# Performance work log

Measured on AMD Instinct MI355X. Metric: run time of the kernel, lower is better.

The kernel has to match this reference:

```python
import jax, jax.numpy as jnp
import numpy as np

N = 100000       # nodes
E = 3200000      # edges (avg degree 32)
IN_C = 64        # in_channels
OUT_C = 10       # out_channels
F = 32           # hidden width of every GCNConv
L = 31           # number of GCNConv layers


def setup_inputs() -> dict:
    key = jax.random.key(0)
    ks = jax.random.split(key, 6)
    x = jax.random.normal(ks[0], (N, IN_C), dtype=jnp.float32)
    edge_index = jax.random.randint(ks[1], (2, E), 0, N, dtype=jnp.int64)
    W1 = jax.random.normal(ks[2], (IN_C, F), dtype=jnp.float32) * 0.1
    b1 = jnp.zeros((F,), dtype=jnp.float32)
    Wc = jax.random.normal(ks[3], (L, F, F), dtype=jnp.float32) * 0.1
    bc = jnp.zeros((L, F), dtype=jnp.float32)
    W2 = jax.random.normal(ks[4], (32 * F, OUT_C), dtype=jnp.float32) * 0.05
    b2 = jnp.zeros((OUT_C,), dtype=jnp.float32)
    return {"x": x, "edge_index": edge_index, "W1": W1, "b1": b1,
            "Wc": Wc, "bc": bc, "W2": W2, "b2": b2}


def mynorm(t):
    mn = t.min(axis=1, keepdims=True)
    mx = t.max(axis=1, keepdims=True)
    return 2.0 * (t - mn) / (mx - mn + 1e-8) - 1.0


def reference(x, edge_index, W1, b1, Wc, bc, W2, b2):
    src, dst = edge_index[0], edge_index[1]
    # GCN symmetric normalization with self-loops: deg = in-degree + 1
    deg = jax.ops.segment_sum(jnp.ones((E,), jnp.float32), dst, num_segments=N) + 1.0
    dis = jax.lax.rsqrt(deg)                       # [N]
    enorm = (dis[src] * dis[dst])[:, None]         # per-edge norm
    snorm = (dis * dis)[:, None]                   # self-loop norm

    def gcn(h, W, b):
        h = h @ W                                  # [N,32]
        agg = jax.ops.segment_sum(h[src] * enorm, dst, num_segments=N)
        return agg + snorm * h + b

    x0 = mynorm(jax.nn.relu(x @ W1 + b1))
    xs = [x0]
    for i in range(L):
        xs.append(gcn(xs[-1], Wc[i], bc[i]))
    norms = [mynorm(t) for t in xs]
    parts = [x0, xs[1]]                            # x0 and xx1 = x1 (raw)
    for i in range(2, 32):
        # quirk in original: index 16 uses raw x16, not a norm difference
        parts.append(xs[16] if i == 16 else norms[i] - norms[i - 2])
    feats = jnp.concatenate(parts, axis=1)         # [N, 32*32]
    return feats @ W2 + b2
```

## Files before the change

### kernel.cpp

```cpp
#include <hip/hip_runtime.h>


#define NB 4
#define BSHIFT 15
#define CSH 9
#define GSLACK 6152

__device__ __forceinline__ float shflx(float v, int m) { return __shfl_xor(v, m, 64); }

__global__ __launch_bounds__(1024) void k_chist(const int* __restrict__ dst, int E,
                                                int* __restrict__ gcnt, int G1) {
    __shared__ int lh[256];
    if (threadIdx.x < 256) lh[threadIdx.x] = 0;
    __syncthreads();
    int chunk = (E + gridDim.x - 1) / gridDim.x;
    int s0 = blockIdx.x * chunk, s1 = min(E, s0 + chunk);
    for (int e = s0 + threadIdx.x; e < s1; e += 1024)
        atomicAdd(&lh[dst[e] >> CSH], 1);
    __syncthreads();
    if (threadIdx.x < G1 && lh[threadIdx.x])
        atomicAdd(&gcnt[threadIdx.x], lh[threadIdx.x]);
}

__global__ void k_cscan(const int* __restrict__ gcnt, int* __restrict__ gptr,
                        int* __restrict__ gcur, int G1, int E) {
    __shared__ int s[256];
    int t = threadIdx.x;
    int v = (t < G1) ? gcnt[t] : 0;
    s[t] = v;
    __syncthreads();
    for (int off = 1; off < 256; off <<= 1) {
        int tv = (t >= off) ? s[t - off] : 0;
        __syncthreads();
        s[t] += tv;
        __syncthreads();
    }
    if (t < G1) { int ex = s[t] - v; gptr[t] = ex; gcur[t] = ex; }
    if (t == 0) gptr[G1] = E;
}

__global__ __launch_bounds__(1024) void k_cscatter(const int* __restrict__ src,
                                                   const int* __restrict__ dst, int E,
                                                   int* __restrict__ gcur,
                                                   int* __restrict__ tmp, int G1) {
    __shared__ int lh[256], lc[256];
    if (threadIdx.x < 256) lh[threadIdx.x] = 0;
    __syncthreads();
    int chunk = (E + gridDim.x - 1) / gridDim.x;
    int s0 = blockIdx.x * chunk, s1 = min(E, s0 + chunk);
    for (int e = s0 + threadIdx.x; e < s1; e += 1024)
        atomicAdd(&lh[dst[e] >> CSH], 1);
    __syncthreads();
    if (threadIdx.x < G1) {
        int c = lh[threadIdx.x];
        lc[threadIdx.x] = c ? atomicAdd(&gcur[threadIdx.x], c) : 0;
    }
    __syncthreads();
    for (int e = s0 + threadIdx.x; e < s1; e += 1024) {
        int d = dst[e];
        int pos = atomicAdd(&lc[d >> CSH], 1);
        tmp[pos] = src[e] | ((d & ((1 << CSH) - 1)) << 17);
    }
}

__global__ __launch_bounds__(256) void k_build(const int* __restrict__ tmp,
                                               const int* __restrict__ gptr,
                                               int* __restrict__ rp4,
                                               int* __restrict__ csr,
                                               float* __restrict__ dis,
                                               int* __restrict__ gend,
                                               int N, int M) {
    __shared__ int h[2048];
    __shared__ int c[2048];
    __shared__ int s[256];
    int g = blockIdx.x;
    int gb = gptr[g], ge = gptr[g + 1];
    int gbP = ((gb + 3) & ~3) + g * GSLACK;
    int t = threadIdx.x;
#pragma unroll
    for (int k = 0; k < 8; ++k) h[t * 8 + k] = 0;
    __syncthreads();
    for (int e = gb + t; e < ge; e += 256) {
        int w = tmp[e];
        int srcv = w & 0x1FFFF, ldst = w >> 17;
        atomicAdd(&h[ldst * NB + (srcv >> BSHIFT)], 1);
    }
    __syncthreads();
    int base8 = t * 8;
    int loc[8], sumP = 0;
#pragma unroll
    for (int k = 0; k < 8; ++k) { loc[k] = h[base8 + k]; sumP += (loc[k] + 3) & ~3; }
    s[t] = sumP;
    __syncthreads();
    for (int off = 1; off < 256; off <<= 1) {
        int tv = (t >= off) ? s[t - off] : 0;
        __syncthreads();
        s[t] += tv;
        __syncthreads();
    }
    int runP = s[t] - sumP;
    int rowbase = g * 2048;
#pragma unroll
    for (int k = 0; k < 8; ++k) {
        int i = base8 + k;
        int abs0 = gbP + runP;
        c[i] = abs0;
        int ig = rowbase + i;
        if (ig <= M) rp4[ig] = abs0;
        int lp = (loc[k] + 3) & ~3;
        for (int j = loc[k]; j < lp; ++j) csr[abs0 + j] = N;
        runP += lp;
    }
    __syncthreads();
    for (int e = gb + t; e < ge; e += 256) {
        int w = tmp[e];
        int srcv = w & 0x1FFFF, ldst = w >> 17;
        int pos = atomicAdd(&c[ldst * NB + (srcv >> BSHIFT)], 1);
        csr[pos] = srcv;
    }
    int nodebase = g << CSH;
    for (int ln = t; ln < (1 << CSH); ln += 256) {
        int n = nodebase + ln;
        if (n < N) {
            int d = h[ln * NB] + h[ln * NB + 1] + h[ln * NB + 2] + h[ln * NB + 3];
            dis[n] = rsqrtf((float)d + 1.0f);
        }
    }
    if (t == 0) gend[g] = gbP + s[255];
    if (g == gridDim.x - 1 && t == 0) rp4[M] = gbP + s[255];
}

__global__ void k_mnorm(const float* __restrict__ W2, float* __restrict__ Mn,
                        float* __restrict__ Rw, float* __restrict__ C0) {
    int idx = blockIdx.x * blockDim.x + threadIdx.x;
    if (idx >= 32 * 32 * 10) return;
    int c = idx % 32, o = (idx / 32) % 10, j = idx / 320;
    float v = 0.f;
    if (j >= 2 && j != 16) v += W2[(32 * j + c) * 10 + o];
    if (j <= 29 && j != 14) v -= W2[(32 * (j + 2) + c) * 10 + o];
    Mn[idx] = v;
    float rw = (j == 0 || j == 1 || j == 16) ? W2[(32 * j + c) * 10 + o] : 0.f;
    Rw[idx] = rw;
    if (j == 0) C0[idx] = v + rw;
}

__global__ __launch_bounds__(256) void k_x0(
    const float* __restrict__ x, const float* __restrict__ W1, const float* __restrict__ b1,
    const float* __restrict__ b2, const float* __restrict__ C0,
    const float* __restrict__ dis, float* __restrict__ hs, float* __restrict__ out, int N)
{
    __shared__ float Wt[32 * 68];
    __shared__ float xs[8 * 64];
    __shared__ float bs[32];
    __shared__ float Cs[10 * 36];
    __shared__ float xmat[8 * 36];
    int t = threadIdx.x;
    for (int i = t; i < 2048; i += 256) {
        int k = i >> 5, cc = i & 31;
        Wt[cc * 68 + k] = W1[i];
    }
    for (int i = t; i < 320; i += 256) {
        int o = i >> 5, cc = i & 31;
        Cs[o * 36 + cc] = C0[i];
    }
    if (t < 32) bs[t] = b1[t];
    if (blockIdx.x == 0 && t < 32) hs[(size_t)N * 32 + t] = 0.f;
    int base = blockIdx.x * 8;
    {
        int nf2 = (min(N - base, 8)) * 32;
        const float2* x2 = (const float2*)(x + (size_t)base * 64);
        float2* xs2 = (float2*)xs;
        for (int i = t; i < nf2; i += 256) xs2[i] = x2[i];
    }
    __syncthreads();

    int node8 = t >> 5, c = t & 31;
    int n = base + node8;
    bool nvalid = (n < N);

    const float4* xs4 = (const float4*)(xs + node8 * 64);
    const float4* Wt4 = (const float4*)(Wt + c * 68);
    float acc = bs[c];
#pragma unroll
    for (int k4 = 0; k4 < 16; ++k4) {
        float4 xv = xs4[k4];
        float4 wv = Wt4[k4];
        acc += xv.x * wv.x + xv.y * wv.y + xv.z * wv.z + xv.w * wv.w;
    }
    acc = fmaxf(acc, 0.f);

    float mn = acc, mx = acc;
#pragma unroll
    for (int m = 1; m <= 16; m <<= 1) { mn = fminf(mn, shflx(mn, m)); mx = fmaxf(mx, shflx(mx, m)); }
    float x0 = 2.f * (acc - mn) / (mx - mn + 1e-8f) - 1.f;
    if (nvalid) {
        float dn = dis[n];
        hs[(size_t)n * 32 + c] = dn * x0;
        xmat[node8 * 36 + c] = x0;
    }
    __syncthreads();

    if (t < 80) {
        int n8 = t / 10, o = t - n8 * 10;
        int no = base + n8;
        if (no < N) {
            const float4* xr = (const float4*)(xmat + n8 * 36);
            const float4* cr = (const float4*)(Cs + o * 36);
            float a = 0.f;
#pragma unroll
            for (int k = 0; k < 8; ++k) {
                float4 xv = xr[k];
                float4 cv = cr[k];
                a += xv.x * cv.x + xv.y * cv.y + xv.z * cv.z + xv.w * cv.w;
            }
            out[(size_t)no * 10 + o] = b2[o] + a;
        }
    }
}

__global__ __launch_bounds__(256) void k_gcn(
    const float4* __restrict__ hs_in, float4* __restrict__ hs_out,
    const float* __restrict__ dis, const int* __restrict__ rp4,
    const int* __restrict__ csr, const int* __restrict__ gend,
    const float* __restrict__ W, const float* __restrict__ b,
    const float* __restrict__ Mn, const float* __restrict__ Rw,
    float* __restrict__ out, int N, int israw)
{
    __shared__ float Ws[1024];
    __shared__ float bs[32];
    __shared__ float Ms[320];
    __shared__ float Rs[320];
    for (int i = threadIdx.x; i < 1024; i += 256) Ws[i] = W[i];
    for (int i = threadIdx.x; i < 320; i += 256) { Ms[i] = Mn[i]; Rs[i] = Rw[i]; }
    if (threadIdx.x < 32) bs[threadIdx.x] = b[threadIdx.x];
    if (blockIdx.x == 0 && threadIdx.x < 8)
        hs_out[(size_t)N * 8 + threadIdx.x] = make_float4(0.f, 0.f, 0.f, 0.f);
    __syncthreads();

    int lane = threadIdx.x & 63;
    int q = lane & 7;
    int i8 = lane >> 3;
    int wave = threadIdx.x >> 6;
    int n = blockIdx.x * 32 + wave * 8 + i8;
    bool valid = (n < N);
    int nn = valid ? n : (N - 1);

    float4 acc = hs_in[(size_t)nn * 8 + q];

    int rbase = nn * NB;
    int rs = rp4[rbase];
    int e3 = ((nn & ((1 << CSH) - 1)) == ((1 << CSH) - 1)) ? gend[nn >> CSH]
                                                          : rp4[rbase + 4];
    const int4* csr4 = (const int4*)csr;
    int4 idx = csr4[rs >> 2];
    for (int p = 0; p < NB; ++p) {
        int re = (p == NB - 1) ? e3 : rp4[rbase + p + 1];
        for (int e = rs; e < re; e += 4) {
            int s0 = idx.x, s1 = idx.y, s2 = idx.z, s3 = idx.w;
            idx = csr4[(e + 4) >> 2];
            float4 v0 = hs_in[(size_t)(s0 * 8 + q)];
            float4 v1 = hs_in[(size_t)(s1 * 8 + q)];
            float4 v2 = hs_in[(size_t)(s2 * 8 + q)];
            float4 v3 = hs_in[(size_t)(s3 * 8 + q)];
            acc.x += v0.x; acc.y += v0.y; acc.z += v0.z; acc.w += v0.w;
            acc.x += v1.x; acc.y += v1.y; acc.z += v1.z; acc.w += v1.w;
            acc.x += v2.x; acc.y += v2.y; acc.z += v2.z; acc.w += v2.w;
            acc.x += v3.x; acc.y += v3.y; acc.z += v3.z; acc.w += v3.w;
        }
        rs = re;
        if (p < NB - 1) __syncthreads();
    }

    float dn = dis[nn];
    float4 g = make_float4(dn * acc.x, dn * acc.y, dn * acc.z, dn * acc.w);

    const float4* W4 = (const float4*)Ws;
    float4 bb = ((const float4*)bs)[q];
    float4 xn = bb;
    int ibase = lane & 0x38;
#pragma unroll
    for (int kp = 0; kp < 8; ++kp) {
        int sl = ibase | kp;
        float gx = __shfl(g.x, sl, 64);
        float gy = __shfl(g.y, sl, 64);
        float gz = __shfl(g.z, sl, 64);
        float gw = __shfl(g.w, sl, 64);
        float4 w0 = W4[(kp * 4 + 0) * 8 + q];
        float4 w1 = W4[(kp * 4 + 1) * 8 + q];
        float4 w2 = W4[(kp * 4 + 2) * 8 + q];
        float4 w3 = W4[(kp * 4 + 3) * 8 + q];
        xn.x += gx * w0.x + gy * w1.x + gz * w2.x + gw * w3.x;
        xn.y += gx * w0.y + gy * w1.y + gz * w2.y + gw * w3.y;
        xn.z += gx * w0.z + gy * w1.z + gz * w2.z + gw * w3.z;
        xn.w += gx * w0.w + gy * w1.w + gz * w2.w + gw * w3.w;
    }

    if (valid)
        hs_out[(size_t)n * 8 + q] = make_float4(dn * xn.x, dn * xn.y, dn * xn.z, dn * xn.w);

    float mn = fminf(fminf(xn.x, xn.y), fminf(xn.z, xn.w));
    float mx = fmaxf(fmaxf(xn.x, xn.y), fmaxf(xn.z, xn.w));
#pragma unroll
    for (int m = 1; m <= 4; m <<= 1) { mn = fminf(mn, shflx(mn, m)); mx = fmaxf(mx, shflx(mx, m)); }
    float sc = 2.f / (mx - mn + 1e-8f);
    float4 nr = make_float4((xn.x - mn) * sc - 1.f, (xn.y - mn) * sc - 1.f,
                            (xn.z - mn) * sc - 1.f, (xn.w - mn) * sc - 1.f);

    const float4* M4 = (const float4*)Ms;
    const float4* R4 = (const float4*)Rs;
    float outA = 0.f, outB = 0.f;
#pragma unroll
    for (int o = 0; o < 10; ++o) {
        float4 m4 = M4[o * 8 + q];
        float t = nr.x * m4.x + nr.y * m4.y + nr.z * m4.z + nr.w * m4.w;
        if (israw) {
            float4 r4 = R4[o * 8 + q];
            t += xn.x * r4.x + xn.y * r4.y + xn.z * r4.z + xn.w * r4.w;
        }
        t += shflx(t, 1); t += shflx(t, 2); t += shflx(t, 4);
        if (o == q) outA = t;
        if (o == 8 + q) outB = t;
    }
    if (valid) {
        out[n * 10 + q] += outA;
        if (q < 2) out[n * 10 + 8 + q] += outB;
    }
}

extern "C" void kernel_launch(void* const* d_in, const int* in_sizes, int n_in,
                              void* d_out, int out_size, void* d_ws, size_t ws_size,
                              hipStream_t stream)
{
    const float* x  = (const float*)d_in[0];
    const int*   ei = (const int*)d_in[1];
    const float* W1 = (const float*)d_in[2];
    const float* b1 = (const float*)d_in[3];
    const float* Wc = (const float*)d_in[4];
    const float* bc = (const float*)d_in[5];
    const float* W2 = (const float*)d_in[6];
    const float* b2 = (const float*)d_in[7];
    float* out = (float*)d_out;

    const int N = in_sizes[0] / 64;
    const int E = in_sizes[1] / 2;
    const int M = N * NB;
    const int G1 = (N + (1 << CSH) - 1) >> CSH;
    const int* src = ei;
    const int* dst = ei + E;

    char* ws = (char*)d_ws;
    size_t off = 0;
    auto alloc = [&](size_t bytes) -> void* {
        void* p = ws + off;
        off = (off + bytes + 255) & ~size_t(255);
        return p;
    };
    int*   gcnt    = (int*)alloc(256 * 4);
    int*   gptr    = (int*)alloc(257 * 4);
    int*   gcur    = (int*)alloc(256 * 4);
    int*   rp4     = (int*)alloc((size_t)(M + 1) * 4);
    float* dis     = (float*)alloc((size_t)N * 4);
    int*   gend    = (int*)alloc(256 * 4);
    int*   tmp     = (int*)alloc((size_t)E * 4);
    int*   csr     = (int*)alloc(((size_t)E + (size_t)G1 * GSLACK + 64) * 4);
    float* hs_a    = (float*)alloc((size_t)(N + 1) * 32 * 4);
    float* hs_b    = (float*)alloc((size_t)(N + 1) * 32 * 4);
    float* Mn      = (float*)alloc(32 * 32 * 10 * 4);
    float* Rw      = (float*)alloc(32 * 32 * 10 * 4);
    float* C0      = (float*)alloc(320 * 4);

    hipMemsetAsync(gcnt, 0, 256 * 4, stream);
    k_chist<<<256, 1024, 0, stream>>>(dst, E, gcnt, G1);
    k_cscan<<<1, 256, 0, stream>>>(gcnt, gptr, gcur, G1, E);
    k_cscatter<<<256, 1024, 0, stream>>>(src, dst, E, gcur, tmp, G1);
    k_build<<<G1, 256, 0, stream>>>(tmp, gptr, rp4, csr, dis, gend, N, M);
    k_mnorm<<<(32 * 32 * 10 + 255) / 256, 256, 0, stream>>>(W2, Mn, Rw, C0);

    const int gb0 = (N + 7) / 8;
    k_x0<<<gb0, 256, 0, stream>>>(x, W1, b1, b2, C0, dis, hs_a, out, N);

    const int gb = (N + 31) / 32;
    float* hin = hs_a; float* hout = hs_b;
    for (int j = 1; j <= 31; ++j) {
        int israw = (j == 1 || j == 16) ? 1 : 0;
        k_gcn<<<gb, 256, 0, stream>>>((const float4*)hin, (float4*)hout, dis, rp4,
                                      csr, gend,
                                      Wc + (size_t)(j - 1) * 1024,
                                      bc + (size_t)(j - 1) * 32,
                                      Mn + (size_t)j * 320,
                                      Rw + (size_t)j * 320,
                                      out, N, israw);
        float* t = hin; hin = hout; hout = t;
    }
}
```

Baseline: 1.879 ms.

## Reorder CSR by source bucket and balance edge gathers across lanes per wave

```diff
diff --git a/kernel.cpp b/kernel.cpp
--- a/kernel.cpp
+++ b/kernel.cpp
@@ -83,7 +83,7 @@
     for (int e = gb + t; e < ge; e += 256) {
         int w = tmp[e];
         int srcv = w & 0x1FFFF, ldst = w >> 17;
-        atomicAdd(&h[ldst * NB + (srcv >> BSHIFT)], 1);
+        atomicAdd(&h[(srcv >> BSHIFT) * (1 << CSH) + ldst], 1);
     }
     __syncthreads();
     int base8 = t * 8;
@@ -105,29 +105,29 @@
         int i = base8 + k;
         int abs0 = gbP + runP;
         c[i] = abs0;
-        int ig = rowbase + i;
-        if (ig <= M) rp4[ig] = abs0;
+        rp4[rowbase + i] = abs0;
         int lp = (loc[k] + 3) & ~3;
-        for (int j = loc[k]; j < lp; ++j) csr[abs0 + j] = N;
+        int lb = i & ((1 << CSH) - 1);
+        int padw = (lb << 17) | N;
+        for (int j = loc[k]; j < lp; ++j) csr[abs0 + j] = padw;
         runP += lp;
     }
     __syncthreads();
     for (int e = gb + t; e < ge; e += 256) {
         int w = tmp[e];
         int srcv = w & 0x1FFFF, ldst = w >> 17;
-        int pos = atomicAdd(&c[ldst * NB + (srcv >> BSHIFT)], 1);
-        csr[pos] = srcv;
+        int pos = atomicAdd(&c[(srcv >> BSHIFT) * (1 << CSH) + ldst], 1);
+        csr[pos] = w;
     }
     int nodebase = g << CSH;
     for (int ln = t; ln < (1 << CSH); ln += 256) {
         int n = nodebase + ln;
         if (n < N) {
-            int d = h[ln * NB] + h[ln * NB + 1] + h[ln * NB + 2] + h[ln * NB + 3];
+            int d = h[ln] + h[512 + ln] + h[1024 + ln] + h[1536 + ln];
             dis[n] = rsqrtf((float)d + 1.0f);
         }
     }
     if (t == 0) gend[g] = gbP + s[255];
-    if (g == gridDim.x - 1 && t == 0) rp4[M] = gbP + s[255];
 }
 
 __global__ void k_mnorm(const float* __restrict__ W2, float* __restrict__ Mn,
@@ -218,6 +218,16 @@
     }
 }
 
+#define FLUSHP() do { if (cur >= 0) { \
+    atomicAdd(&wsc[wave][cur][(q << 2)    ], part.x); \
+    atomicAdd(&wsc[wave][cur][(q << 2) + 1], part.y); \
+    atomicAdd(&wsc[wave][cur][(q << 2) + 2], part.z); \
+    atomicAdd(&wsc[wave][cur][(q << 2) + 3], part.w); } } while (0)
+#define EDGE(wrd) do { int slot = ((wrd) >> 17) - l0; \
+    if (slot != cur) { FLUSHP(); cur = slot; part = make_float4(0.f, 0.f, 0.f, 0.f); } \
+    float4 v = hs_in[(size_t)((((wrd) & 0x1FFFF)) * 8 + q)]; \
+    part.x += v.x; part.y += v.y; part.z += v.z; part.w += v.w; } while (0)
+
 __global__ __launch_bounds__(256) void k_gcn(
     const float4* __restrict__ hs_in, float4* __restrict__ hs_out,
     const float* __restrict__ dis, const int* __restrict__ rp4,
@@ -230,9 +240,11 @@
     __shared__ float bs[32];
     __shared__ float Ms[320];
     __shared__ float Rs[320];
+    __shared__ float wsc[4][8][32];
     for (int i = threadIdx.x; i < 1024; i += 256) Ws[i] = W[i];
     for (int i = threadIdx.x; i < 320; i += 256) { Ms[i] = Mn[i]; Rs[i] = Rw[i]; }
     if (threadIdx.x < 32) bs[threadIdx.x] = b[threadIdx.x];
+    ((float4*)wsc)[threadIdx.x] = make_float4(0.f, 0.f, 0.f, 0.f);
     if (blockIdx.x == 0 && threadIdx.x < 8)
         hs_out[(size_t)N * 8 + threadIdx.x] = make_float4(0.f, 0.f, 0.f, 0.f);
     __syncthreads();
@@ -245,34 +257,44 @@
     bool valid = (n < N);
     int nn = valid ? n : (N - 1);
 
+    int n0 = blockIdx.x * 32 + wave * 8;
+    int g = n0 >> CSH;
+    int l0 = n0 & ((1 << CSH) - 1);
+    int gb2048 = g << 11;
+    const int4* csr4 = (const int4*)csr;
+
+    int cur = -1;
+    float4 part = make_float4(0.f, 0.f, 0.f, 0.f);
+    for (int p = 0; p < NB; ++p) {
+        int S = rp4[gb2048 + (p << CSH) + l0];
+        int T = (l0 + 8 == (1 << CSH) && p == NB - 1)
+                    ? gend[g]
+                    : rp4[gb2048 + (p << CSH) + l0 + 8];
+        int Q = (T - S) >> 2;
+        int qlo = (Q * i8) >> 3, qhi = (Q * (i8 + 1)) >> 3;
+        int qb = (S >> 2) + qlo, qe = (S >> 2) + qhi;
+        if (qb < qe) {
+            int4 wq = csr4[qb];
+            for (int qd = qb; qd < qe; ++qd) {
+                int4 nx;
+                if (qd + 1 < qe) nx = csr4[qd + 1];
+                EDGE(wq.x); EDGE(wq.y); EDGE(wq.z); EDGE(wq.w);
+                wq = nx;
+            }
+        }
+        if (p < NB - 1) __syncthreads();
+    }
+    FLUSHP();
+    __syncthreads();
+
     float4 acc = hs_in[(size_t)nn * 8 + q];
-
-    int rbase = nn * NB;
-    int rs = rp4[rbase];
-    int e3 = ((nn & ((1 << CSH) - 1)) == ((1 << CSH) - 1)) ? gend[nn >> CSH]
-                                                          : rp4[rbase + 4];
-    const int4* csr4 = (const int4*)csr;
-    int4 idx = csr4[rs >> 2];
-    for (int p = 0; p < NB; ++p) {
-        int re = (p == NB - 1) ? e3 : rp4[rbase + p + 1];
-        for (int e = rs; e < re; e += 4) {
-            int s0 = idx.x, s1 = idx.y, s2 = idx.z, s3 = idx.w;
-            idx = csr4[(e + 4) >> 2];
-            float4 v0 = hs_in[(size_t)(s0 * 8 + q)];
-            float4 v1 = hs_in[(size_t)(s1 * 8 + q)];
-            float4 v2 = hs_in[(size_t)(s2 * 8 + q)];
-            float4 v3 = hs_in[(size_t)(s3 * 8 + q)];
-            acc.x += v0.x; acc.y += v0.y; acc.z += v0.z; acc.w += v0.w;
-            acc.x += v1.x; acc.y += v1.y; acc.z += v1.z; acc.w += v1.w;
-            acc.x += v2.x; acc.y += v2.y; acc.z += v2.z; acc.w += v2.w;
-            acc.x += v3.x; acc.y += v3.y; acc.z += v3.z; acc.w += v3.w;
-        }
-        rs = re;
-        if (p < NB - 1) __syncthreads();
+    {
+        float4 sv = *(const float4*)&wsc[wave][i8][q << 2];
+        acc.x += sv.x; acc.y += sv.y; acc.z += sv.z; acc.w += sv.w;
     }
 
     float dn = dis[nn];
-    float4 g = make_float4(dn * acc.x, dn * acc.y, dn * acc.z, dn * acc.w);
+    float4 g4 = make_float4(dn * acc.x, dn * acc.y, dn * acc.z, dn * acc.w);
 
     const float4* W4 = (const float4*)Ws;
     float4 bb = ((const float4*)bs)[q];
@@ -281,10 +303,10 @@
 #pragma unroll
     for (int kp = 0; kp < 8; ++kp) {
         int sl = ibase | kp;
-        float gx = __shfl(g.x, sl, 64);
-        float gy = __shfl(g.y, sl, 64);
-        float gz = __shfl(g.z, sl, 64);
-        float gw = __shfl(g.w, sl, 64);
+        float gx = __shfl(g4.x, sl, 64);
+        float gy = __shfl(g4.y, sl, 64);
+        float gz = __shfl(g4.z, sl, 64);
+        float gw = __shfl(g4.w, sl, 64);
         float4 w0 = W4[(kp * 4 + 0) * 8 + q];
         float4 w1 = W4[(kp * 4 + 1) * 8 + q];
         float4 w2 = W4[(kp * 4 + 2) * 8 + q];
@@ -358,7 +380,7 @@
     int*   gcnt    = (int*)alloc(256 * 4);
     int*   gptr    = (int*)alloc(257 * 4);
     int*   gcur    = (int*)alloc(256 * 4);
-    int*   rp4     = (int*)alloc((size_t)(M + 1) * 4);
+    int*   rp4     = (int*)alloc(((size_t)G1 * 2048 + 8) * 4);
     float* dis     = (float*)alloc((size_t)N * 4);
     int*   gend    = (int*)alloc(256 * 4);
     int*   tmp     = (int*)alloc((size_t)E * 4);
```

After: 3.316 ms. +76.4%, slower.
